# Performance work log

Hardware: AMD Instinct MI355X
Metric: run time of the kernel (lower is better)

## Reference

```python
import jax, jax.numpy as jnp
import numpy as np

D_MODEL = 1024
N_HEADS = 16
HEAD_DIM = D_MODEL // N_HEADS
WINDOW = 256


def setup_inputs() -> dict:
    key = jax.random.key(0)
    k1, k2, k3 = jax.random.split(key, 3)
    x = jax.random.normal(k1, (1, 4096, D_MODEL), dtype=jnp.float32)
    # torch nn.Linear weights: [out_features, in_features]
    W_qkv = jax.random.normal(k2, (3 * D_MODEL, D_MODEL), dtype=jnp.float32) * (D_MODEL ** -0.5)
    W_proj = jax.random.normal(k3, (D_MODEL, D_MODEL), dtype=jnp.float32) * (D_MODEL ** -0.5)
    return {"x": x, "W_qkv": W_qkv, "W_proj": W_proj}


def reference(x, W_qkv, W_proj):
    B, T, D = x.shape
    H, Hd = N_HEADS, HEAD_DIM
    qkv = (x @ W_qkv.T).reshape(B, T, 3, H, Hd)
    qkv = jnp.transpose(qkv, (2, 0, 3, 1, 4))  # [3, B, H, T, Hd]
    q, k, v = qkv[0], qkv[1], qkv[2]
    # causal + sliding-window mask: allowed iff 0 <= i - j < WINDOW
    i = jnp.arange(T)[:, None]
    j = jnp.arange(T)[None, :]
    mask = (j <= i) & (j >= i - (WINDOW - 1))  # [T, T] bool
    scale = Hd ** -0.5
    attn = jnp.einsum('bhid,bhjd->bhij', q, k) * scale
    attn = jnp.where(mask, attn, -jnp.inf)
    attn = jax.nn.softmax(attn, axis=-1)
    out = jnp.einsum('bhij,bhjd->bhid', attn, v)  # [B, H, T, Hd]
    out = jnp.transpose(out, (0, 2, 1, 3)).reshape(B, T, D)
    return out @ W_proj.T
```

## Files before the change

### kernel.cpp

```cpp
#include <hip/hip_runtime.h>
#include <hip/hip_bf16.h>


#define T_SEQ   4096
#define DM      1024
#define NH      16
#define HD      64
#define WIN     256

typedef unsigned short u16_t;
typedef u16_t  u16v8 __attribute__((ext_vector_type(8)));
typedef __bf16 bf16v8 __attribute__((ext_vector_type(8)));
typedef float  f32v4 __attribute__((ext_vector_type(4)));

__device__ __forceinline__ f32v4 mfma_bf16(u16v8 a, u16v8 b, f32v4 c) {
    return __builtin_amdgcn_mfma_f32_16x16x32_bf16(
        __builtin_bit_cast(bf16v8, a), __builtin_bit_cast(bf16v8, b), c, 0, 0, 0);
}

__device__ __forceinline__ u16_t f2bf(float f) {
    unsigned u = __builtin_bit_cast(unsigned, f);
    u += 0x7fffu + ((u >> 16) & 1u);
    return (u16_t)(u >> 16);
}

__device__ __forceinline__ float exp2_fast(float x) {
    return __builtin_amdgcn_exp2f(x);
}

__device__ __forceinline__ void gload_lds16(const u16_t* g, u16_t* l) {
    __builtin_amdgcn_global_load_lds(
        (const __attribute__((address_space(1))) unsigned int*)g,
        (__attribute__((address_space(3))) unsigned int*)l, 16, 0, 0);
}

__global__ void cvt_kernel(const float* __restrict__ in, u16_t* __restrict__ out, int n8) {
    int i = blockIdx.x * blockDim.x + threadIdx.x;
    if (i >= n8) return;
    const float4* p = (const float4*)(in + (size_t)i * 8);
    float4 a = p[0], b = p[1];
    u16v8 o;
    o[0] = f2bf(a.x); o[1] = f2bf(a.y); o[2] = f2bf(a.z); o[3] = f2bf(a.w);
    o[4] = f2bf(b.x); o[5] = f2bf(b.y); o[6] = f2bf(b.z); o[7] = f2bf(b.w);
    *(u16v8*)(out + (size_t)i * 8) = o;
}

template <typename OutT>
__global__ __launch_bounds__(256) void gemm_bt(const u16_t* __restrict__ A,
                                               const u16_t* __restrict__ B,
                                               OutT* __restrict__ C,
                                               int M, int N, int K) {
    __shared__ u16_t lA[128 * 32];
    __shared__ u16_t lB[128 * 32];
    const int tid = threadIdx.x;
    const int l  = tid & 63;
    const int w  = tid >> 6;
    const int lr = l & 15, ko = l >> 4;
    const int wr = (w >> 1) * 64, wc = (w & 1) * 64;
    const int arow0 = blockIdx.y * 128, bcol0 = blockIdx.x * 128;

    f32v4 acc[4][4];
#pragma unroll
    for (int m = 0; m < 4; ++m)
#pragma unroll
        for (int n = 0; n < 4; ++n) acc[m][n] = f32v4{0.f, 0.f, 0.f, 0.f};

    const int s0 = tid, s1 = tid + 256;
    const int r0 = s0 >> 2, g0 = s0 & 3;
    const int r1 = s1 >> 2, g1 = s1 & 3;
    const int k0q = (g0 ^ ((r0 >> 1) & 3)) * 8;
    const int k1q = (g1 ^ ((r1 >> 1) & 3)) * 8;

    for (int kt = 0; kt < K; kt += 32) {
        __syncthreads();
        gload_lds16(A + (size_t)(arow0 + r0) * K + kt + k0q, lA + s0 * 8);
        gload_lds16(A + (size_t)(arow0 + r1) * K + kt + k1q, lA + s1 * 8);
        gload_lds16(B + (size_t)(bcol0 + r0) * K + kt + k0q, lB + s0 * 8);
        gload_lds16(B + (size_t)(bcol0 + r1) * K + kt + k1q, lB + s1 * 8);
        __syncthreads();

        u16v8 af[4], bfv[4];
#pragma unroll
        for (int m = 0; m < 4; ++m) {
            int row = wr + m * 16 + lr;
            af[m] = *(const u16v8*)(lA + row * 32 + (ko ^ ((row >> 1) & 3)) * 8);
        }
#pragma unroll
        for (int n = 0; n < 4; ++n) {
            int row = wc + n * 16 + lr;
            bfv[n] = *(const u16v8*)(lB + row * 32 + (ko ^ ((row >> 1) & 3)) * 8);
        }
#pragma unroll
        for (int m = 0; m < 4; ++m)
#pragma unroll
            for (int n = 0; n < 4; ++n)
                acc[m][n] = mfma_bf16(af[m], bfv[n], acc[m][n]);
    }

#pragma unroll
    for (int m = 0; m < 4; ++m) {
        int crow0 = arow0 + wr + m * 16 + ko * 4;
#pragma unroll
        for (int n = 0; n < 4; ++n) {
            int ccol = bcol0 + wc + n * 16 + lr;
#pragma unroll
            for (int j = 0; j < 4; ++j) {
                float v = acc[m][n][j];
                if constexpr (sizeof(OutT) == 2)
                    C[(size_t)(crow0 + j) * N + ccol] = (OutT)f2bf(v);
                else
                    C[(size_t)(crow0 + j) * N + ccol] = (OutT)v;
            }
        }
    }
}

__global__ __launch_bounds__(256) void vtrans_kernel(const u16_t* __restrict__ qkv,
                                                     u16_t* __restrict__ vt) {
    __shared__ u16_t tile[64][72];
    const int t0 = blockIdx.x * 64, h = blockIdx.y;
    const int tid = threadIdx.x;
    {
        int r = tid >> 2, c = (tid & 3) * 16;
        const u16_t* src = qkv + (size_t)(t0 + r) * (3 * DM) + 2 * DM + h * HD + c;
        *(u16v8*)&tile[r][c]     = *(const u16v8*)src;
        *(u16v8*)&tile[r][c + 8] = *(const u16v8*)(src + 8);
    }
    __syncthreads();
    {
        int d = tid >> 2, ts = (tid & 3) * 16;
        u16_t* dst = vt + ((size_t)h * HD + d) * T_SEQ + t0 + ts;
        u16v8 o0, o1;
#pragma unroll
        for (int i = 0; i < 8; ++i) { o0[i] = tile[ts + i][d]; o1[i] = tile[ts + 8 + i][d]; }
        *(u16v8*)dst       = o0;
        *(u16v8*)(dst + 8) = o1;
    }
}

__global__ __launch_bounds__(256) void attn_kernel(const u16_t* __restrict__ qkv,
                                                   const u16_t* __restrict__ vt,
                                                   u16_t* __restrict__ out) {
    __shared__ u16_t lK[2][64 * 64];
    __shared__ u16_t lV[2][64 * 64];
    __shared__ u16_t pbuf[4][16 * 64];

    const int h = blockIdx.y;
    const int q0 = blockIdx.x * 64;
    const int tid = threadIdx.x;
    const int w = tid >> 6, l = tid & 63;
    const int lr = l & 15, g = l >> 4;
    const int i0 = q0 + w * 16;
    u16_t* P = pbuf[w];

    const int r_st = tid >> 3;
    const int c8l  = tid & 7;
    const u16_t* kBase = qkv + DM + h * HD;
    const u16_t* vBase = vt + (size_t)h * HD * T_SEQ;

    u16v8 qf0, qf1;
    {
        const u16_t* qrow = qkv + h * HD + (size_t)(i0 + lr) * (3 * DM) + g * 8;
        qf0 = *(const u16v8*)qrow;
        qf1 = *(const u16v8*)(qrow + 32);
    }

    f32v4 o[4];
#pragma unroll
    for (int n = 0; n < 4; ++n) o[n] = f32v4{0.f, 0.f, 0.f, 0.f};
    float m_run[4], l_run[4];
#pragma unroll
    for (int j = 0; j < 4; ++j) { m_run[j] = -1e30f; l_run[j] = 0.f; }

    const int c0 = (q0 >= WIN) ? q0 - WIN : 0;
    const int nch = ((q0 - c0) >> 6) + 1;

#define STAGE_KV(buf, cc)                                                              \
    do {                                                                               \
        _Pragma("unroll")                                                              \
        for (int p = 0; p < 2; ++p) {                                                  \
            int rr = r_st + p * 32;                                                    \
            int cs = c8l ^ (rr & 7);                                                   \
            gload_lds16(kBase + (size_t)(cc + rr) * (3 * DM) + cs * 8,                 \
                        lK[buf] + (size_t)(rr * 64 + c8l * 8));                        \
            gload_lds16(vBase + (size_t)rr * T_SEQ + (cc) + cs * 8,                    \
                        lV[buf] + (size_t)(rr * 64 + c8l * 8));                        \
        }                                                                              \
    } while (0)

    STAGE_KV(0, c0);

    const float sc = 0.125f * 1.4426950408889634f;

    for (int ci = 0; ci < nch; ++ci) {
        const int c = c0 + (ci << 6);
        const int cur = ci & 1;
        __syncthreads();
        if (ci + 1 < nch) STAGE_KV(cur ^ 1, c + 64);

        const u16_t* K = lK[cur];
        const u16_t* V = lV[cur];

        f32v4 s[4];
#pragma unroll
        for (int kt = 0; kt < 4; ++kt) {
            int krow = kt * 16 + lr;
            u16v8 k0 = *(const u16v8*)(K + krow * 64 + ((g     ^ (krow & 7)) * 8));
            u16v8 k1 = *(const u16v8*)(K + krow * 64 + (((4+g) ^ (krow & 7)) * 8));
            f32v4 z = f32v4{0.f, 0.f, 0.f, 0.f};
            z = mfma_bf16(qf0, k0, z);
            z = mfma_bf16(qf1, k1, z);
            s[kt] = z;
        }

        const bool full = (c + 63 <= i0) && (c >= i0 - 240);
        if (full) {
#pragma unroll
            for (int kt = 0; kt < 4; ++kt)
#pragma unroll
                for (int j = 0; j < 4; ++j) s[kt][j] *= sc;
        } else {
#pragma unroll
            for (int j = 0; j < 4; ++j) {
                const int i = i0 + g * 4 + j;
#pragma unroll
                for (int kt = 0; kt < 4; ++kt) {
                    const int jg = c + kt * 16 + lr;
                    float v = s[kt][j] * sc;
                    const bool okm = (jg <= i) && (jg >= i - (WIN - 1));
                    s[kt][j] = okm ? v : -3e38f;
                }
            }
        }

        float mloc[4], corr[4], rsum[4];
#pragma unroll
        for (int j = 0; j < 4; ++j)
            mloc[j] = fmaxf(fmaxf(s[0][j], s[1][j]), fmaxf(s[2][j], s[3][j]));
#pragma unroll
        for (int d = 1; d < 16; d <<= 1)
#pragma unroll
            for (int j = 0; j < 4; ++j) mloc[j] = fmaxf(mloc[j], __shfl_xor(mloc[j], d, 64));
#pragma unroll
        for (int j = 0; j < 4; ++j) {
            float mnew = fmaxf(m_run[j], mloc[j]);
            corr[j] = exp2_fast(m_run[j] - mnew);
            m_run[j] = mnew;
            rsum[j] = 0.f;
        }
#pragma unroll
        for (int kt = 0; kt < 4; ++kt)
#pragma unroll
            for (int j = 0; j < 4; ++j) {
                float p = exp2_fast(s[kt][j] - m_run[j]);
                rsum[j] += p;
                int rP = g * 4 + j;
                int col = kt * 16 + lr;
                int c8 = col >> 3;
                P[rP * 64 + ((c8 ^ (rP & 7)) * 8 + (col & 7))] = f2bf(p);
            }
#pragma unroll
        for (int d = 1; d < 16; d <<= 1)
#pragma unroll
            for (int j = 0; j < 4; ++j) rsum[j] += __shfl_xor(rsum[j], d, 64);
#pragma unroll
        for (int j = 0; j < 4; ++j) l_run[j] = l_run[j] * corr[j] + rsum[j];
#pragma unroll
        for (int n = 0; n < 4; ++n)
#pragma unroll
            for (int j = 0; j < 4; ++j) o[n][j] *= corr[j];

        u16v8 pa0 = *(const u16v8*)(P + lr * 64 + ((g     ^ (lr & 7)) * 8));
        u16v8 pa1 = *(const u16v8*)(P + lr * 64 + (((4+g) ^ (lr & 7)) * 8));
#pragma unroll
        for (int n = 0; n < 4; ++n) {
            int vrow = n * 16 + lr;
            u16v8 v0 = *(const u16v8*)(V + vrow * 64 + ((g     ^ (vrow & 7)) * 8));
            u16v8 v1 = *(const u16v8*)(V + vrow * 64 + (((4+g) ^ (vrow & 7)) * 8));
            o[n] = mfma_bf16(pa0, v0, o[n]);
            o[n] = mfma_bf16(pa1, v1, o[n]);
        }
    }
#undef STAGE_KV

#pragma unroll
    for (int n = 0; n < 4; ++n)
#pragma unroll
        for (int j = 0; j < 4; ++j) {
            int t = i0 + g * 4 + j;
            out[(size_t)t * DM + h * HD + n * 16 + lr] = f2bf(o[n][j] / l_run[j]);
        }
}

extern "C" void kernel_launch(void* const* d_in, const int* in_sizes, int n_in,
                              void* d_out, int out_size, void* d_ws, size_t ws_size,
                              hipStream_t stream) {
    const float* x     = (const float*)d_in[0];
    const float* wqkv  = (const float*)d_in[1];
    const float* wproj = (const float*)d_in[2];
    float* out = (float*)d_out;
    char* ws = (char*)d_ws;

    u16_t* xb     = (u16_t*)(ws);
    u16_t* wqkvb  = (u16_t*)(ws + (size_t)(8u << 20));
    u16_t* wprojb = (u16_t*)(ws + (size_t)(14u << 20));
    u16_t* qkvb   = (u16_t*)(ws + (size_t)(16u << 20));
    u16_t* vt     = (u16_t*)(ws + (size_t)(40u << 20));
    u16_t* attnb  = (u16_t*)(ws);

    const int n8x = T_SEQ * DM / 8, n8q = 3 * DM * DM / 8, n8p = DM * DM / 8;
    cvt_kernel<<<(n8x + 255) / 256, 256, 0, stream>>>(x, xb, n8x);
    cvt_kernel<<<(n8q + 255) / 256, 256, 0, stream>>>(wqkv, wqkvb, n8q);
    cvt_kernel<<<(n8p + 255) / 256, 256, 0, stream>>>(wproj, wprojb, n8p);

    gemm_bt<u16_t><<<dim3(3 * DM / 128, T_SEQ / 128), 256, 0, stream>>>(
        xb, wqkvb, qkvb, T_SEQ, 3 * DM, DM);

    vtrans_kernel<<<dim3(T_SEQ / 64, NH), 256, 0, stream>>>(qkvb, vt);

    attn_kernel<<<dim3(T_SEQ / 64, NH), 256, 0, stream>>>(qkvb, vt, attnb);

    gemm_bt<float><<<dim3(DM / 128, T_SEQ / 128), 256, 0, stream>>>(
        attnb, wprojb, out, T_SEQ, DM, DM);
}
```

Measured before the change: 175.0 us.

## Replace GEMM with double-buffered 8-wave kernel using K=64 tiles and phased MFMA

```diff
diff --git a/kernel.cpp b/kernel.cpp
--- a/kernel.cpp
+++ b/kernel.cpp
@@ -45,67 +45,159 @@
     *(u16v8*)(out + (size_t)i * 8) = o;
 }
 
-template <typename OutT>
-__global__ __launch_bounds__(256) void gemm_bt(const u16_t* __restrict__ A,
-                                               const u16_t* __restrict__ B,
-                                               OutT* __restrict__ C,
-                                               int M, int N, int K) {
-    __shared__ u16_t lA[128 * 32];
-    __shared__ u16_t lB[128 * 32];
+template <int BM, int BN, int WN, int WAVES, typename OutT>
+__global__ __launch_bounds__(WAVES * 64, 2)
+void gemm8p(const u16_t* __restrict__ A, const u16_t* __restrict__ B,
+            OutT* __restrict__ C, int M, int N, int K) {
+    constexpr int WM  = WAVES / WN;
+    constexpr int PWM = BM / WM;
+    constexpr int PWN = BN / WN;
+    constexpr int M_F = PWM / 16, N_F = PWN / 16;
+    constexpr int A_H = M_F / 2, N_H = N_F / 2;
+    constexpr int THREADS = WAVES * 64;
+    constexpr int RPP = THREADS / 8;
+
+    __shared__ u16_t lA[2][BM * 64];
+    __shared__ u16_t lB[2][BN * 64];
+
     const int tid = threadIdx.x;
-    const int l  = tid & 63;
-    const int w  = tid >> 6;
-    const int lr = l & 15, ko = l >> 4;
-    const int wr = (w >> 1) * 64, wc = (w & 1) * 64;
-    const int arow0 = blockIdx.y * 128, bcol0 = blockIdx.x * 128;
-
-    f32v4 acc[4][4];
-#pragma unroll
-    for (int m = 0; m < 4; ++m)
-#pragma unroll
-        for (int n = 0; n < 4; ++n) acc[m][n] = f32v4{0.f, 0.f, 0.f, 0.f};
-
-    const int s0 = tid, s1 = tid + 256;
-    const int r0 = s0 >> 2, g0 = s0 & 3;
-    const int r1 = s1 >> 2, g1 = s1 & 3;
-    const int k0q = (g0 ^ ((r0 >> 1) & 3)) * 8;
-    const int k1q = (g1 ^ ((r1 >> 1) & 3)) * 8;
-
-    for (int kt = 0; kt < K; kt += 32) {
+    const int l = tid & 63, w = tid >> 6;
+    const int lr = l & 15, g = l >> 4;
+    const int wrh = w / WN, wcq = w % WN;
+    const int arow0 = blockIdx.y * BM, bcol0 = blockIdx.x * BN;
+    const int r_st = tid >> 3, c8l = tid & 7;
+    const int NT = K >> 6;
+
+    f32v4 acc[M_F][N_F];
+#pragma unroll
+    for (int m = 0; m < M_F; ++m)
+#pragma unroll
+        for (int n = 0; n < N_F; ++n) acc[m][n] = f32v4{0.f, 0.f, 0.f, 0.f};
+
+#define GSTAGE(buf, kt0)                                                                \
+    do {                                                                                \
+        _Pragma("unroll")                                                               \
+        for (int p = 0; p < BM / RPP; ++p) {                                            \
+            int rr = r_st + p * RPP;                                                    \
+            int cs = (c8l ^ (rr & 7)) * 8;                                              \
+            gload_lds16(A + (size_t)(arow0 + rr) * K + (kt0) + cs,                      \
+                        lA[buf] + (size_t)(rr * 64 + c8l * 8));                         \
+        }                                                                               \
+        _Pragma("unroll")                                                               \
+        for (int p = 0; p < BN / RPP; ++p) {                                            \
+            int rr = r_st + p * RPP;                                                    \
+            int cs = (c8l ^ (rr & 7)) * 8;                                              \
+            gload_lds16(B + (size_t)(bcol0 + rr) * K + (kt0) + cs,                      \
+                        lB[buf] + (size_t)(rr * 64 + c8l * 8));                         \
+        }                                                                               \
+    } while (0)
+
+#define SBAR  do { __builtin_amdgcn_s_barrier(); __builtin_amdgcn_sched_barrier(0); } while (0)
+
+    GSTAGE(0, 0);
+    __syncthreads();
+
+    u16v8 af[A_H][2], bfr[N_F][2];
+
+    for (int t = 0; t < NT; ++t) {
+        const int cur = t & 1;
+        const u16_t* cA = lA[cur];
+        const u16_t* cB = lB[cur];
+        const bool pre = (t + 1 < NT);
+
+        if (pre) GSTAGE(cur ^ 1, (t + 1) << 6);
+#pragma unroll
+        for (int mf = 0; mf < A_H; ++mf) {
+            int row = wrh * PWM + mf * 16 + lr;
+#pragma unroll
+            for (int ks = 0; ks < 2; ++ks)
+                af[mf][ks] = *(const u16v8*)(cA + row * 64 + (((ks * 4 + g) ^ (row & 7)) * 8));
+        }
+#pragma unroll
+        for (int nf = 0; nf < N_H; ++nf) {
+            int row = wcq * PWN + nf * 16 + lr;
+#pragma unroll
+            for (int ks = 0; ks < 2; ++ks)
+                bfr[nf][ks] = *(const u16v8*)(cB + row * 64 + (((ks * 4 + g) ^ (row & 7)) * 8));
+        }
+        SBAR;
+        __builtin_amdgcn_s_setprio(1);
+#pragma unroll
+        for (int mf = 0; mf < A_H; ++mf)
+#pragma unroll
+            for (int nf = 0; nf < N_H; ++nf)
+#pragma unroll
+                for (int ks = 0; ks < 2; ++ks)
+                    acc[mf][nf] = mfma_bf16(af[mf][ks], bfr[nf][ks], acc[mf][nf]);
+        __builtin_amdgcn_s_setprio(0);
+        __builtin_amdgcn_sched_barrier(0);
+        SBAR;
+
+#pragma unroll
+        for (int nf = N_H; nf < N_F; ++nf) {
+            int row = wcq * PWN + nf * 16 + lr;
+#pragma unroll
+            for (int ks = 0; ks < 2; ++ks)
+                bfr[nf][ks] = *(const u16v8*)(cB + row * 64 + (((ks * 4 + g) ^ (row & 7)) * 8));
+        }
+        SBAR;
+        __builtin_amdgcn_s_setprio(1);
+#pragma unroll
+        for (int mf = 0; mf < A_H; ++mf)
+#pragma unroll
+            for (int nf = N_H; nf < N_F; ++nf)
+#pragma unroll
+                for (int ks = 0; ks < 2; ++ks)
+                    acc[mf][nf] = mfma_bf16(af[mf][ks], bfr[nf][ks], acc[mf][nf]);
+        __builtin_amdgcn_s_setprio(0);
+        __builtin_amdgcn_sched_barrier(0);
+        SBAR;
+
+#pragma unroll
+        for (int mf = 0; mf < A_H; ++mf) {
+            int row = wrh * PWM + (A_H + mf) * 16 + lr;
+#pragma unroll
+            for (int ks = 0; ks < 2; ++ks)
+                af[mf][ks] = *(const u16v8*)(cA + row * 64 + (((ks * 4 + g) ^ (row & 7)) * 8));
+        }
+        SBAR;
+        __builtin_amdgcn_s_setprio(1);
+#pragma unroll
+        for (int mf = 0; mf < A_H; ++mf)
+#pragma unroll
+            for (int nf = N_H; nf < N_F; ++nf)
+#pragma unroll
+                for (int ks = 0; ks < 2; ++ks)
+                    acc[A_H + mf][nf] = mfma_bf16(af[mf][ks], bfr[nf][ks], acc[A_H + mf][nf]);
+        __builtin_amdgcn_s_setprio(0);
+        __builtin_amdgcn_sched_barrier(0);
+        SBAR;
+
+        __builtin_amdgcn_s_setprio(1);
+#pragma unroll
+        for (int mf = 0; mf < A_H; ++mf)
+#pragma unroll
+            for (int nf = 0; nf < N_H; ++nf)
+#pragma unroll
+                for (int ks = 0; ks < 2; ++ks)
+                    acc[A_H + mf][nf] = mfma_bf16(af[mf][ks], bfr[nf][ks], acc[A_H + mf][nf]);
+        __builtin_amdgcn_s_setprio(0);
+        __builtin_amdgcn_sched_barrier(0);
+        if (pre) { asm volatile("s_waitcnt vmcnt(0)" ::: "memory"); }
         __syncthreads();
-        gload_lds16(A + (size_t)(arow0 + r0) * K + kt + k0q, lA + s0 * 8);
-        gload_lds16(A + (size_t)(arow0 + r1) * K + kt + k1q, lA + s1 * 8);
-        gload_lds16(B + (size_t)(bcol0 + r0) * K + kt + k0q, lB + s0 * 8);
-        gload_lds16(B + (size_t)(bcol0 + r1) * K + kt + k1q, lB + s1 * 8);
-        __syncthreads();
-
-        u16v8 af[4], bfv[4];
-#pragma unroll
-        for (int m = 0; m < 4; ++m) {
-            int row = wr + m * 16 + lr;
-            af[m] = *(const u16v8*)(lA + row * 32 + (ko ^ ((row >> 1) & 3)) * 8);
-        }
-#pragma unroll
-        for (int n = 0; n < 4; ++n) {
-            int row = wc + n * 16 + lr;
-            bfv[n] = *(const u16v8*)(lB + row * 32 + (ko ^ ((row >> 1) & 3)) * 8);
-        }
-#pragma unroll
-        for (int m = 0; m < 4; ++m)
-#pragma unroll
-            for (int n = 0; n < 4; ++n)
-                acc[m][n] = mfma_bf16(af[m], bfv[n], acc[m][n]);
-    }
-
-#pragma unroll
-    for (int m = 0; m < 4; ++m) {
-        int crow0 = arow0 + wr + m * 16 + ko * 4;
-#pragma unroll
-        for (int n = 0; n < 4; ++n) {
-            int ccol = bcol0 + wc + n * 16 + lr;
+    }
+#undef GSTAGE
+#undef SBAR
+
+#pragma unroll
+    for (int mf = 0; mf < M_F; ++mf) {
+        int crow0 = arow0 + wrh * PWM + mf * 16 + g * 4;
+#pragma unroll
+        for (int nf = 0; nf < N_F; ++nf) {
+            int ccol = bcol0 + wcq * PWN + nf * 16 + lr;
 #pragma unroll
             for (int j = 0; j < 4; ++j) {
-                float v = acc[m][n][j];
+                float v = acc[mf][nf][j];
                 if constexpr (sizeof(OutT) == 2)
                     C[(size_t)(crow0 + j) * N + ccol] = (OutT)f2bf(v);
                 else
@@ -164,7 +256,6 @@
         qf0 = *(const u16v8*)qrow;
         qf1 = *(const u16v8*)(qrow + 32);
     }
-
     f32v4 o[4];
 #pragma unroll
     for (int n = 0; n < 4; ++n) o[n] = f32v4{0.f, 0.f, 0.f, 0.f};
@@ -313,13 +404,13 @@
     cvt_kernel<<<(n8q + 255) / 256, 256, 0, stream>>>(wqkv, wqkvb, n8q);
     cvt_kernel<<<(n8p + 255) / 256, 256, 0, stream>>>(wproj, wprojb, n8p);
 
-    gemm_bt<u16_t><<<dim3(3 * DM / 128, T_SEQ / 128), 256, 0, stream>>>(
+    gemm8p<256, 256, 4, 8, u16_t><<<dim3(3 * DM / 256, T_SEQ / 256), 512, 0, stream>>>(
         xb, wqkvb, qkvb, T_SEQ, 3 * DM, DM);
 
     vtrans_kernel<<<dim3(T_SEQ / 64, NH), 256, 0, stream>>>(qkvb, vt);
 
     attn_kernel<<<dim3(T_SEQ / 64, NH), 256, 0, stream>>>(qkvb, vt, attnb);
 
-    gemm_bt<float><<<dim3(DM / 128, T_SEQ / 128), 256, 0, stream>>>(
+    gemm8p<128, 128, 2, 4, float><<<dim3(DM / 128, T_SEQ / 128), 256, 0, stream>>>(
         attnb, wprojb, out, T_SEQ, DM, DM);
 }
```

New measurement: 179.6 us. 1.03x slower.
